# Optimization experiments

Measured on AMD Instinct MI355X. Metric: run time of the kernel, lower is better.

Reference implementation:

```python
import jax, jax.numpy as jnp
import numpy as np

B, T, N, F_, KH, D, KD = 16, 12, 325, 64, 4, 16, 3  # batch, time, nodes, feat, heads, head_dim, diffusion steps
H = KH // 2
EPS = 1e-5


def setup_inputs() -> dict:
    key = jax.random.key(0)
    ks = jax.random.split(key, 16)
    lin = lambda k: (jax.random.normal(k, (F_, F_), jnp.float32) * 0.02)
    return {
        "x": jax.random.normal(ks[0], (B, T, N, F_), jnp.float32),
        "A": jax.random.uniform(ks[1], (KD, N, N), jnp.float32),
        "AT": jax.random.uniform(ks[2], (KD, N, N), jnp.float32),
        "Wq": lin(ks[3]), "bq": jnp.zeros((F_,), jnp.float32),
        "Wk": lin(ks[4]), "bk": jnp.zeros((F_,), jnp.float32),
        "Wks": lin(ks[5]), "bks": jnp.zeros((F_,), jnp.float32),
        "Wv": lin(ks[6]), "bv": jnp.zeros((F_,), jnp.float32),
        "Wvs": lin(ks[7]), "bvs": jnp.zeros((F_,), jnp.float32),
        "Wdi": jax.random.normal(ks[8], (H, KD, N, N), jnp.float32) * 0.05,
        "Wdo": jax.random.normal(ks[9], (H, KD, N, N), jnp.float32) * 0.05,
        "Wf1": lin(ks[10]), "bf1": jnp.zeros((F_,), jnp.float32),
        "Wf2": lin(ks[11]), "bf2": jnp.zeros((F_,), jnp.float32),
        "g_ln": jnp.ones((F_,), jnp.float32), "b_ln": jnp.zeros((F_,), jnp.float32),
    }


def _heads(y):
    # [B,T,N,F] -> [KH,B,T,N,D]  (torch.split along -1 then stack on dim 0)
    return y.reshape(B, T, N, KH, D).transpose(3, 0, 1, 2, 4)


def _attn_half(q, k, ks_, v, vs, bias):
    # q,k,ks_,v,vs: [H,B,T,N,D]; bias: [H,1,1,N,N]
    scale = 1.0 / jnp.sqrt(jnp.float32(D))
    e = jnp.einsum('hbtnd,hbtmd->hbtnm', q, k) * scale + bias
    es = jax.nn.sigmoid((q * ks_).sum(-1, keepdims=True) * scale)  # [H,B,T,N,1]
    e = e - e.max(-1, keepdims=True)
    ex = jnp.exp(e)
    a = ex / (es + ex.sum(-1, keepdims=True))  # sigmoid-augmented softmax
    out = jnp.einsum('hbtnm,hbtmd->hbtnd', a, v)
    return out + vs - a.sum(-1, keepdims=True) * vs


def reference(x, A, AT, Wq, bq, Wk, bk, Wks, bks, Wv, bv, Wvs, bvs,
              Wdi, Wdo, Wf1, bf1, Wf2, bf2, g_ln, b_ln):
    q = _heads(x @ Wq.T + bq)
    k = _heads(x @ Wk.T + bk)
    ks_ = _heads(x @ Wks.T + bks)
    v = _heads(x @ Wv.T + bv)
    vs = _heads(x @ Wvs.T + bvs)

    # DCN graph-diffusion bias: sum_j W[h,j] * A[j] -> [H,1,1,N,N]
    bias_i = jnp.einsum('hknm,knm->hnm', Wdi, A)[:, None, None]
    bias_o = jnp.einsum('hknm,knm->hnm', Wdo, AT)[:, None, None]

    vi = _attn_half(q[:H], k[:H], ks_[:H], v[:H], vs[:H], bias_i)
    vo = _attn_half(q[H:], k[H:], ks_[H:], v[H:], vs[H:], bias_o)

    val = jnp.concatenate([vi, vo], 0)  # [KH,B,T,N,D]
    val = val.transpose(1, 2, 3, 0, 4).reshape(B, T, N, F_)

    h = jax.nn.gelu(val @ Wf1.T + bf1, approximate=False) @ Wf2.T + bf2
    h = h + x

    mu = h.mean(-1, keepdims=True)
    var = ((h - mu) ** 2).mean(-1, keepdims=True)
    return g_ln * (h - mu) / jnp.sqrt(var + EPS) + b_ln
```

## Files before the change

kernel.cpp:

```cpp
#include <hip/hip_runtime.h>
#include <hip/hip_bf16.h>
#include <math.h>

#define NN 325
#define FD 64
#define KH 4
#define DH 16
#define BT 192
#define NN2 (NN*NN)
#define PST (NN*DH)
#define SSTR 340
#define BSTR 352
#define VTS  352
#define VSLICE (16*VTS)
#define HSTR 72
#define NPROJ 975
#define NBIAS ((KH*NN*BSTR + 255)/256)
#define NPAD  (KH*BT)
#define LOG2E 1.44269504088896f

typedef __attribute__((ext_vector_type(8))) short short8;
typedef __attribute__((ext_vector_type(4))) float f32x4;

union U8 { uint4 u; short8 s; ushort us[8]; };
__device__ inline short8 lds8(const ushort* p){ U8 t; t.u = *(const uint4*)p; return t.s; }
__device__ inline float b2f(ushort v){ return __uint_as_float(((unsigned)v) << 16); }
__device__ inline ushort f2b(float f){
  unsigned u = __float_as_uint(f);
  u += 0x7fff + ((u >> 16) & 1);
  return (ushort)(u >> 16);
}
__device__ inline unsigned pk2(float a, float b){
  union { __hip_bfloat162 h; unsigned u; } t;
  t.h = __float22bfloat162_rn(float2{a, b});
  return t.u;
}
__device__ inline short8 cvt8(const float* p){
  float4 u = ((const float4*)p)[0], v = ((const float4*)p)[1];
  U8 t;
  t.us[0]=f2b(u.x); t.us[1]=f2b(u.y); t.us[2]=f2b(u.z); t.us[3]=f2b(u.w);
  t.us[4]=f2b(v.x); t.us[5]=f2b(v.y); t.us[6]=f2b(v.z); t.us[7]=f2b(v.w);
  return t.s;
}

__global__ __launch_bounds__(256) void wpack_kernel(
    const float* __restrict__ Wq,  const float* __restrict__ bq,
    const float* __restrict__ Wk,  const float* __restrict__ bk,
    const float* __restrict__ Wks, const float* __restrict__ bks,
    const float* __restrict__ Wv,  const float* __restrict__ bv,
    const float* __restrict__ Wvs, const float* __restrict__ bvs,
    const float* __restrict__ Wf1, const float* __restrict__ Wf2,
    ushort* __restrict__ Wcat, float* __restrict__ bcat){
  int blk = blockIdx.x;
  const float* Ws[7] = {Wq, Wk, Wks, Wv, Wvs, Wf1, Wf2};
  const float* bs[5] = {bq, bk, bks, bv, bvs};
  int f = blk * 64 + (threadIdx.x >> 2);
  int c0 = (threadIdx.x & 3) * 8;
  const float* wr = Ws[blk] + (f & 63) * 64;
  unsigned* dst = (unsigned*)Wcat + f * 32 + c0;
  #pragma unroll
  for (int c = 0; c < 8; ++c)
    dst[c] = f2b(wr[2*(c0+c)]) | ((unsigned)f2b(wr[2*(c0+c)+1]) << 16);
  if (blk < 5 && (threadIdx.x & 3) == 0) bcat[f] = bs[blk][f & 63];
}

__global__ __launch_bounds__(256) void prep_kernel(
    const float* __restrict__ x, const ushort* __restrict__ Wcat,
    const float* __restrict__ bcat, ushort* __restrict__ proj,
    ushort* __restrict__ vt,
    const float* __restrict__ Wdi, const float* __restrict__ Wdo,
    const float* __restrict__ A,   const float* __restrict__ AT,
    float* __restrict__ biasP){
  int bid = blockIdx.x, tid = threadIdx.x;
  if (bid < NPROJ){
    int lane = tid & 63, wid = tid >> 6;
    int r0 = bid * 64 + wid * 16;
    int m = lane & 15, g = lane >> 4;
    int gr = r0 + m;
    int bt = gr / NN, n = gr - bt * NN;
    const float* xr = x + (size_t)gr * 64 + g * 8;
    short8 xb0 = cvt8(xr);
    short8 xb1 = cvt8(xr + 32);
    for (int ct = 0; ct < 20; ++ct){
      short8 w0 = lds8(Wcat + ((size_t)(ct*16 + m) * 64 + g * 8));
      short8 w1 = lds8(Wcat + ((size_t)(ct*16 + m) * 64 + g * 8 + 32));
      float4 b4 = *(const float4*)(bcat + ct*16 + 4*g);
      f32x4 acc = {b4.x, b4.y, b4.z, b4.w};
      acc = __builtin_amdgcn_mfma_f32_16x16x32_bf16(w0, xb0, acc, 0, 0, 0);
      acc = __builtin_amdgcn_mfma_f32_16x16x32_bf16(w1, xb1, acc, 0, 0, 0);
      if (ct >= 12 && ct < 16){
        ushort* vs = vt + (size_t)((ct-12)*BT + bt) * VSLICE + n;
        #pragma unroll
        for (int rg = 0; rg < 4; ++rg)
          vs[(size_t)(4*g + rg) * VTS] = f2b(acc[rg]);
      } else {
        float sc = (ct < 4) ? 0.25f * LOG2E : 1.0f;
        uint2 w;
        w.x = pk2(acc[0]*sc, acc[1]*sc);
        w.y = pk2(acc[2]*sc, acc[3]*sc);
        *(uint2*)(proj + ((size_t)ct * BT + bt) * PST + n*16 + 4*g) = w;
      }
    }
  } else if (bid < NPROJ + NBIAS){
    int idx = (bid - NPROJ) * 256 + tid;
    if (idx >= KH * NN * BSTR) return;
    int h = idx / (NN * BSTR), rem = idx - h * (NN * BSTR);
    int n = rem / BSTR, m = rem - n * BSTR;
    float s = -1e30f;
    if (m < NN){
      int r = n * NN + m;
      s = 0.f;
      if (h < 2){
        #pragma unroll
        for (int k = 0; k < 3; ++k) s += Wdi[(h*3 + k)*NN2 + r] * A[k*NN2 + r];
      } else {
        int h2 = h - 2;
        #pragma unroll
        for (int k = 0; k < 3; ++k) s += Wdo[(h2*3 + k)*NN2 + r] * AT[k*NN2 + r];
      }
      s *= LOG2E;
    }
    biasP[idx] = s;
  } else {
    int slice = bid - NPROJ - NBIAS;
    ushort* vs = vt + (size_t)slice * VSLICE;
    if (tid < 432){
      int d = tid / 27, c = NN + tid % 27;
      vs[(size_t)d * VTS + c] = 0;
    }
  }
}

__global__ __launch_bounds__(256, 4) void attn_kernel(
    const ushort* __restrict__ proj, const float* __restrict__ biasP,
    const ushort* __restrict__ vt, ushort* __restrict__ val){
  __shared__ float S[16 * SSTR];
  __shared__ float part[4][16][16];
  __shared__ float rstat[16][2];
  int bhid = blockIdx.x, qt = blockIdx.y;
  int h = bhid / BT, bt = bhid - h * BT;
  int tid = threadIdx.x, lane = tid & 63, wid = tid >> 6;
  const ushort* qb  = proj + (size_t)((0*KH + h)*BT + bt) * PST;
  const ushort* kb  = proj + (size_t)((1*KH + h)*BT + bt) * PST;
  const ushort* ksb = proj + (size_t)((2*KH + h)*BT + bt) * PST;
  const ushort* vsb = proj + (size_t)((4*KH + h)*BT + bt) * PST;
  const ushort* vtg = vt + (size_t)(h*BT + bt) * VSLICE;

  int m = lane & 15, g = lane >> 4;
  short8 zero = {0,0,0,0,0,0,0,0};

  short8 aq = (g < 2) ? lds8(qb + ((size_t)(qt*16 + m) * 16 + g * 8)) : zero;
  short8 kf[6];
  #pragma unroll
  for (int i = 0; i < 6; ++i){
    int ct = wid + 4*i;
    kf[i] = (ct < 21 && g < 2) ? lds8(kb + ((size_t)(ct*16 + m) * 16 + g * 8)) : zero;
  }
  short8 vf[3];
  #pragma unroll
  for (int i = 0; i < 3; ++i){
    int tt = wid + 4*i;
    vf[i] = (tt < 11) ? lds8(vtg + (size_t)m * VTS + tt*32 + g*8) : zero;
  }
  int r = tid >> 4, c = tid & 15;
  int n = qt * 16 + r;
  int nb = min(n, NN - 1);
  const float* bp = biasP + (size_t)(h*NN + nb) * BSTR;
  float4 b4[6];
  #pragma unroll
  for (int j = 0; j < 6; ++j){
    int m0 = c * 4 + 64 * j;
    b4[j] = (m0 < 336) ? *(const float4*)(bp + m0) : make_float4(0.f,0.f,0.f,0.f);
  }
  float qv  = b2f(qb[(size_t)nb * 16 + c]);
  float kv  = b2f(ksb[(size_t)nb * 16 + c]);
  float vsv = b2f(vsb[(size_t)nb * 16 + c]);

  #pragma unroll
  for (int i = 0; i < 6; ++i){
    int ct = wid + 4*i;
    if (ct < 21){
      f32x4 acc = {0.f, 0.f, 0.f, 0.f};
      acc = __builtin_amdgcn_mfma_f32_16x16x32_bf16(aq, kf[i], acc, 0, 0, 0);
      #pragma unroll
      for (int rg = 0; rg < 4; ++rg)
        S[(g*4 + rg)*SSTR + ct*16 + m] = acc[rg];
    }
  }
  __syncthreads();

  {
    float* sr = S + r * SSTR;
    ushort* pr = (ushort*)sr;
    float sum = 0.f;
    #pragma unroll
    for (int j = 0; j < 6; ++j){
      int m0 = c * 4 + 64 * j;
      if (m0 < 336){
        float4 s4 = *(const float4*)(sr + m0);
        float e0 = __builtin_amdgcn_exp2f(s4.x + b4[j].x);
        float e1 = __builtin_amdgcn_exp2f(s4.y + b4[j].y);
        float e2 = __builtin_amdgcn_exp2f(s4.z + b4[j].z);
        float e3 = __builtin_amdgcn_exp2f(s4.w + b4[j].w);
        sum += (e0 + e1) + (e2 + e3);
        uint2 w;
        w.x = pk2(e0, e1);
        w.y = pk2(e2, e3);
        *(uint2*)(pr + m0) = w;
      }
    }
    float dp = qv * kv;
    dp += __shfl_xor(dp, 1, 64); dp += __shfl_xor(dp, 2, 64);
    dp += __shfl_xor(dp, 4, 64); dp += __shfl_xor(dp, 8, 64);
    sum += __shfl_xor(sum, 1, 64); sum += __shfl_xor(sum, 2, 64);
    sum += __shfl_xor(sum, 4, 64); sum += __shfl_xor(sum, 8, 64);
    if (c == 0){
      float esv = __builtin_amdgcn_rcpf(1.f + __builtin_amdgcn_exp2f(-dp));
      float iv  = __builtin_amdgcn_rcpf(esv + sum);
      rstat[r][0] = iv; rstat[r][1] = 1.f - sum * iv;
    }
  }
  __syncthreads();

  {
    const ushort* prow = (const ushort*)S + (size_t)m * (SSTR * 2);
    f32x4 acc = {0.f, 0.f, 0.f, 0.f};
    #pragma unroll
    for (int i = 0; i < 3; ++i){
      int tt = wid + 4*i;
      if (tt < 11){
        short8 ap = (tt == 10 && g >= 2) ? zero : lds8(prow + tt*32 + g*8);
        acc = __builtin_amdgcn_mfma_f32_16x16x32_bf16(ap, vf[i], acc, 0, 0, 0);
      }
    }
    #pragma unroll
    for (int rg = 0; rg < 4; ++rg)
      part[wid][g*4 + rg][m] = acc[rg];
  }
  __syncthreads();

  if (n < NN){
    float s = part[0][r][c] + part[1][r][c] + part[2][r][c] + part[3][r][c];
    float res = s * rstat[r][0] + rstat[r][1] * vsv;
    val[((size_t)bt * NN + n) * FD + h * 16 + c] = f2b(res);
  }
}

__global__ __launch_bounds__(256) void ffn_kernel(
    const ushort* __restrict__ val, const float* __restrict__ x,
    const ushort* __restrict__ Wf1b, const float* __restrict__ bf1,
    const ushort* __restrict__ Wf2b, const float* __restrict__ bf2,
    const float* __restrict__ g_ln, const float* __restrict__ b_ln,
    float* __restrict__ out){
  __shared__ ushort hs[4][16 * HSTR];
  int tid = threadIdx.x, lane = tid & 63, wid = tid >> 6;
  int m = lane & 15, g = lane >> 4;
  int r0 = blockIdx.x * 64 + wid * 16;
  int row = r0 + m;

  short8 vb0 = lds8(val + ((size_t)row * 64 + g * 8));
  short8 vb1 = lds8(val + ((size_t)row * 64 + g * 8 + 32));

  #pragma unroll
  for (int ct = 0; ct < 4; ++ct){
    short8 w0 = lds8(Wf1b + ((size_t)(ct*16 + m) * 64 + g * 8));
    short8 w1 = lds8(Wf1b + ((size_t)(ct*16 + m) * 64 + g * 8 + 32));
    float4 b4 = *(const float4*)(bf1 + ct*16 + 4*g);
    f32x4 acc = {b4.x, b4.y, b4.z, b4.w};
    acc = __builtin_amdgcn_mfma_f32_16x16x32_bf16(w0, vb0, acc, 0, 0, 0);
    acc = __builtin_amdgcn_mfma_f32_16x16x32_bf16(w1, vb1, acc, 0, 0, 0);
    uint2 w;
    float g0 = 0.5f*acc[0]*(1.f + erff(acc[0]*0.70710678118654752f));
    float g1 = 0.5f*acc[1]*(1.f + erff(acc[1]*0.70710678118654752f));
    float g2 = 0.5f*acc[2]*(1.f + erff(acc[2]*0.70710678118654752f));
    float g3 = 0.5f*acc[3]*(1.f + erff(acc[3]*0.70710678118654752f));
    w.x = pk2(g0, g1); w.y = pk2(g2, g3);
    *(uint2*)&hs[wid][m * HSTR + ct*16 + 4*g] = w;
  }
  asm volatile("s_waitcnt lgkmcnt(0)" ::: "memory");
  short8 h0 = lds8(&hs[wid][m * HSTR + g * 8]);
  short8 h1 = lds8(&hs[wid][m * HSTR + g * 8 + 32]);

  float t[4][4];
  #pragma unroll
  for (int ct = 0; ct < 4; ++ct){
    short8 w0 = lds8(Wf2b + ((size_t)(ct*16 + m) * 64 + g * 8));
    short8 w1 = lds8(Wf2b + ((size_t)(ct*16 + m) * 64 + g * 8 + 32));
    float4 b4 = *(const float4*)(bf2 + ct*16 + 4*g);
    f32x4 acc = {b4.x, b4.y, b4.z, b4.w};
    acc = __builtin_amdgcn_mfma_f32_16x16x32_bf16(w0, h0, acc, 0, 0, 0);
    acc = __builtin_amdgcn_mfma_f32_16x16x32_bf16(w1, h1, acc, 0, 0, 0);
    float4 xr = *(const float4*)(x + (size_t)row * 64 + ct*16 + 4*g);
    t[ct][0] = acc[0] + xr.x; t[ct][1] = acc[1] + xr.y;
    t[ct][2] = acc[2] + xr.z; t[ct][3] = acc[3] + xr.w;
  }
  float s = 0.f;
  #pragma unroll
  for (int ct = 0; ct < 4; ++ct) s += (t[ct][0]+t[ct][1]) + (t[ct][2]+t[ct][3]);
  s += __shfl_xor(s, 16, 64); s += __shfl_xor(s, 32, 64);
  float mu = s * (1.f/64.f);
  float v = 0.f;
  #pragma unroll
  for (int ct = 0; ct < 4; ++ct){
    #pragma unroll
    for (int rg = 0; rg < 4; ++rg){ float d = t[ct][rg] - mu; v += d*d; }
  }
  v += __shfl_xor(v, 16, 64); v += __shfl_xor(v, 32, 64);
  float rs = rsqrtf(v * (1.f/64.f) + 1e-5f);
  #pragma unroll
  for (int ct = 0; ct < 4; ++ct){
    float4 g4 = *(const float4*)(g_ln + ct*16 + 4*g);
    float4 bb = *(const float4*)(b_ln + ct*16 + 4*g);
    float4 o;
    o.x = g4.x*(t[ct][0]-mu)*rs + bb.x;
    o.y = g4.y*(t[ct][1]-mu)*rs + bb.y;
    o.z = g4.z*(t[ct][2]-mu)*rs + bb.z;
    o.w = g4.w*(t[ct][3]-mu)*rs + bb.w;
    *(float4*)(out + (size_t)row * 64 + ct*16 + 4*g) = o;
  }
}

extern "C" void kernel_launch(void* const* d_in, const int* in_sizes, int n_in,
                              void* d_out, int out_size, void* d_ws, size_t ws_size,
                              hipStream_t stream) {
  const float* x    = (const float*)d_in[0];
  const float* A    = (const float*)d_in[1];
  const float* AT   = (const float*)d_in[2];
  const float* Wq   = (const float*)d_in[3];
  const float* bq   = (const float*)d_in[4];
  const float* Wk   = (const float*)d_in[5];
  const float* bk   = (const float*)d_in[6];
  const float* Wks  = (const float*)d_in[7];
  const float* bks  = (const float*)d_in[8];
  const float* Wv   = (const float*)d_in[9];
  const float* bv   = (const float*)d_in[10];
  const float* Wvs  = (const float*)d_in[11];
  const float* bvs  = (const float*)d_in[12];
  const float* Wdi  = (const float*)d_in[13];
  const float* Wdo  = (const float*)d_in[14];
  const float* Wf1  = (const float*)d_in[15];
  const float* bf1  = (const float*)d_in[16];
  const float* Wf2  = (const float*)d_in[17];
  const float* bf2  = (const float*)d_in[18];
  const float* g_ln = (const float*)d_in[19];
  const float* b_ln = (const float*)d_in[20];
  float* out = (float*)d_out;

  float* ws = (float*)d_ws;
  ushort* proj  = (ushort*)ws;
  float*  biasP = ws + 9984000;
  ushort* val   = (ushort*)(ws + 10441600);
  ushort* vt    = (ushort*)(ws + 12438400);
  ushort* Wcat  = (ushort*)(ws + 14601088);
  float*  bcat  = ws + 14615424;
  ushort* Wf1b  = Wcat + 320*64;
  ushort* Wf2b  = Wcat + 384*64;

  wpack_kernel<<<7, 256, 0, stream>>>(Wq, bq, Wk, bk, Wks, bks,
                                      Wv, bv, Wvs, bvs, Wf1, Wf2, Wcat, bcat);
  prep_kernel<<<NPROJ + NBIAS + NPAD, 256, 0, stream>>>(
      x, Wcat, bcat, proj, vt, Wdi, Wdo, A, AT, biasP);
  attn_kernel<<<dim3(KH*BT, 21), 256, 0, stream>>>(proj, biasP, vt, val);
  ffn_kernel<<<975, 256, 0, stream>>>(val, x, Wf1b, bf1, Wf2b, bf2,
                                      g_ln, b_ln, out);
}
```

Measured before the change: 198.1 us.

## Rewrite attention as single-wave blocks with transposed bias and compacted projections

The attention kernel goes from four waves per block, with three barriers and a cross-wave reduction, to one 64-thread wave per block. That wave loops over all 21 key tiles, applies exp2 to the MFMA output in registers, writes bf16 probabilities to LDS and keeps row sums in registers. The diffusion bias is now written transposed (336x336 per head) through a shared-memory tile transpose, so each lane reads a float4 that matches its MFMA output layout. The projection buffer also drops the unused value slots, which shrinks the workspace. The aim is to remove barrier and LDS round-trip overhead. The cost is less parallelism per block, serial per-wave loops, and K and V loaded directly from global memory inside the loop.

```diff
diff --git a/kernel.cpp b/kernel.cpp
--- a/kernel.cpp
+++ b/kernel.cpp
@@ -9,13 +9,14 @@
 #define BT 192
 #define NN2 (NN*NN)
 #define PST (NN*DH)
-#define SSTR 340
-#define BSTR 352
+#define BTN 336
+#define BTH (336*336)
 #define VTS  352
 #define VSLICE (16*VTS)
+#define PSTR 344
 #define HSTR 72
 #define NPROJ 975
-#define NBIAS ((KH*NN*BSTR + 255)/256)
+#define NBIAS 144
 #define NPAD  (KH*BT)
 #define LOG2E 1.44269504088896f
 
@@ -70,7 +71,8 @@
     ushort* __restrict__ vt,
     const float* __restrict__ Wdi, const float* __restrict__ Wdo,
     const float* __restrict__ A,   const float* __restrict__ AT,
-    float* __restrict__ biasP){
+    float* __restrict__ biasT){
+  __shared__ float tile[64 * 65];
   int bid = blockIdx.x, tid = threadIdx.x;
   if (bid < NPROJ){
     int lane = tid & 63, wid = tid >> 6;
@@ -94,33 +96,51 @@
         for (int rg = 0; rg < 4; ++rg)
           vs[(size_t)(4*g + rg) * VTS] = f2b(acc[rg]);
       } else {
+        int slot = (ct < 12) ? ct : ct - 4;
         float sc = (ct < 4) ? 0.25f * LOG2E : 1.0f;
         uint2 w;
         w.x = pk2(acc[0]*sc, acc[1]*sc);
         w.y = pk2(acc[2]*sc, acc[3]*sc);
-        *(uint2*)(proj + ((size_t)ct * BT + bt) * PST + n*16 + 4*g) = w;
+        *(uint2*)(proj + ((size_t)slot * BT + bt) * PST + n*16 + 4*g) = w;
       }
     }
   } else if (bid < NPROJ + NBIAS){
-    int idx = (bid - NPROJ) * 256 + tid;
-    if (idx >= KH * NN * BSTR) return;
-    int h = idx / (NN * BSTR), rem = idx - h * (NN * BSTR);
-    int n = rem / BSTR, m = rem - n * BSTR;
-    float s = -1e30f;
-    if (m < NN){
-      int r = n * NN + m;
-      s = 0.f;
-      if (h < 2){
-        #pragma unroll
-        for (int k = 0; k < 3; ++k) s += Wdi[(h*3 + k)*NN2 + r] * A[k*NN2 + r];
-      } else {
-        int h2 = h - 2;
-        #pragma unroll
-        for (int k = 0; k < 3; ++k) s += Wdo[(h2*3 + k)*NN2 + r] * AT[k*NN2 + r];
+    int tb = bid - NPROJ;
+    int h = tb / 36, rem = tb - h * 36;
+    int nt = rem / 6, mt = rem - nt * 6;
+    int n0 = nt * 64, m0 = mt * 64;
+    #pragma unroll
+    for (int i = 0; i < 16; ++i){
+      int idx = i * 256 + tid;
+      int nn = idx >> 6, mm = idx & 63;
+      int n = n0 + nn, mc = m0 + mm;
+      float s;
+      if (mc >= NN) s = -1e30f;
+      else if (n >= NN) s = 0.f;
+      else {
+        int r = n * NN + mc;
+        s = 0.f;
+        if (h < 2){
+          #pragma unroll
+          for (int k = 0; k < 3; ++k) s += Wdi[(h*3 + k)*NN2 + r] * A[k*NN2 + r];
+        } else {
+          int h2 = h - 2;
+          #pragma unroll
+          for (int k = 0; k < 3; ++k) s += Wdo[(h2*3 + k)*NN2 + r] * AT[k*NN2 + r];
+        }
+        s *= LOG2E;
       }
-      s *= LOG2E;
-    }
-    biasP[idx] = s;
+      tile[mm * 65 + nn] = s;
+    }
+    __syncthreads();
+    #pragma unroll
+    for (int i = 0; i < 16; ++i){
+      int idx = i * 256 + tid;
+      int mm = idx >> 6, nn = idx & 63;
+      int gm = m0 + mm, gn = n0 + nn;
+      if (gm < BTN && gn < BTN)
+        biasT[(size_t)h * BTH + (size_t)gm * BTN + gn] = tile[mm * 65 + nn];
+    }
   } else {
     int slice = bid - NPROJ - NBIAS;
     ushort* vs = vt + (size_t)slice * VSLICE;
@@ -131,118 +151,81 @@
   }
 }
 
-__global__ __launch_bounds__(256, 4) void attn_kernel(
-    const ushort* __restrict__ proj, const float* __restrict__ biasP,
+__global__ __launch_bounds__(64) void attn_kernel(
+    const ushort* __restrict__ proj, const float* __restrict__ biasT,
     const ushort* __restrict__ vt, ushort* __restrict__ val){
-  __shared__ float S[16 * SSTR];
-  __shared__ float part[4][16][16];
-  __shared__ float rstat[16][2];
+  __shared__ ushort P[16 * PSTR];
   int bhid = blockIdx.x, qt = blockIdx.y;
   int h = bhid / BT, bt = bhid - h * BT;
-  int tid = threadIdx.x, lane = tid & 63, wid = tid >> 6;
-  const ushort* qb  = proj + (size_t)((0*KH + h)*BT + bt) * PST;
-  const ushort* kb  = proj + (size_t)((1*KH + h)*BT + bt) * PST;
-  const ushort* ksb = proj + (size_t)((2*KH + h)*BT + bt) * PST;
-  const ushort* vsb = proj + (size_t)((4*KH + h)*BT + bt) * PST;
+  int lane = threadIdx.x & 63;
+  int m = lane & 15, g = lane >> 4;
+  const ushort* qb  = proj + (size_t)(( 0 + h)*BT + bt) * PST;
+  const ushort* kb  = proj + (size_t)(( 4 + h)*BT + bt) * PST;
+  const ushort* ksb = proj + (size_t)(( 8 + h)*BT + bt) * PST;
+  const ushort* vsb = proj + (size_t)((12 + h)*BT + bt) * PST;
   const ushort* vtg = vt + (size_t)(h*BT + bt) * VSLICE;
-
-  int m = lane & 15, g = lane >> 4;
   short8 zero = {0,0,0,0,0,0,0,0};
 
   short8 aq = (g < 2) ? lds8(qb + ((size_t)(qt*16 + m) * 16 + g * 8)) : zero;
-  short8 kf[6];
-  #pragma unroll
-  for (int i = 0; i < 6; ++i){
-    int ct = wid + 4*i;
-    kf[i] = (ct < 21 && g < 2) ? lds8(kb + ((size_t)(ct*16 + m) * 16 + g * 8)) : zero;
-  }
-  short8 vf[3];
-  #pragma unroll
-  for (int i = 0; i < 3; ++i){
-    int tt = wid + 4*i;
-    vf[i] = (tt < 11) ? lds8(vtg + (size_t)m * VTS + tt*32 + g*8) : zero;
-  }
-  int r = tid >> 4, c = tid & 15;
-  int n = qt * 16 + r;
-  int nb = min(n, NN - 1);
-  const float* bp = biasP + (size_t)(h*NN + nb) * BSTR;
-  float4 b4[6];
-  #pragma unroll
-  for (int j = 0; j < 6; ++j){
-    int m0 = c * 4 + 64 * j;
-    b4[j] = (m0 < 336) ? *(const float4*)(bp + m0) : make_float4(0.f,0.f,0.f,0.f);
-  }
-  float qv  = b2f(qb[(size_t)nb * 16 + c]);
-  float kv  = b2f(ksb[(size_t)nb * 16 + c]);
-  float vsv = b2f(vsb[(size_t)nb * 16 + c]);
-
-  #pragma unroll
-  for (int i = 0; i < 6; ++i){
-    int ct = wid + 4*i;
-    if (ct < 21){
-      f32x4 acc = {0.f, 0.f, 0.f, 0.f};
-      acc = __builtin_amdgcn_mfma_f32_16x16x32_bf16(aq, kf[i], acc, 0, 0, 0);
-      #pragma unroll
-      for (int rg = 0; rg < 4; ++rg)
-        S[(g*4 + rg)*SSTR + ct*16 + m] = acc[rg];
-    }
-  }
-  __syncthreads();
-
-  {
-    float* sr = S + r * SSTR;
-    ushort* pr = (ushort*)sr;
-    float sum = 0.f;
+  float qv[4], kv[4], vsv[4];
+  #pragma unroll
+  for (int rg = 0; rg < 4; ++rg){
+    int nn = min(qt*16 + g*4 + rg, NN - 1);
+    qv[rg]  = b2f(qb [(size_t)nn * 16 + m]);
+    kv[rg]  = b2f(ksb[(size_t)nn * 16 + m]);
+    vsv[rg] = b2f(vsb[(size_t)nn * 16 + m]);
+  }
+
+  const float* bTc = biasT + (size_t)h * BTH + qt*16 + g*4;
+  float sm[4] = {0.f, 0.f, 0.f, 0.f};
+  for (int ct = 0; ct < 21; ++ct){
+    int col = ct*16 + m;
+    short8 kf = (g < 2) ? lds8(kb + ((size_t)col * 16 + g * 8)) : zero;
+    f32x4 s = {0.f, 0.f, 0.f, 0.f};
+    s = __builtin_amdgcn_mfma_f32_16x16x32_bf16(aq, kf, s, 0, 0, 0);
+    float4 b4 = *(const float4*)(bTc + (size_t)col * BTN);
+    float e0 = __builtin_amdgcn_exp2f(s[0] + b4.x);
+    float e1 = __builtin_amdgcn_exp2f(s[1] + b4.y);
+    float e2 = __builtin_amdgcn_exp2f(s[2] + b4.z);
+    float e3 = __builtin_amdgcn_exp2f(s[3] + b4.w);
+    sm[0] += e0; sm[1] += e1; sm[2] += e2; sm[3] += e3;
+    P[(g*4 + 0) * PSTR + col] = f2b(e0);
+    P[(g*4 + 1) * PSTR + col] = f2b(e1);
+    P[(g*4 + 2) * PSTR + col] = f2b(e2);
+    P[(g*4 + 3) * PSTR + col] = f2b(e3);
+  }
+
+  float dp[4];
+  #pragma unroll
+  for (int rg = 0; rg < 4; ++rg) dp[rg] = qv[rg] * kv[rg];
+  #pragma unroll
+  for (int o = 1; o <= 8; o <<= 1){
     #pragma unroll
-    for (int j = 0; j < 6; ++j){
-      int m0 = c * 4 + 64 * j;
-      if (m0 < 336){
-        float4 s4 = *(const float4*)(sr + m0);
-        float e0 = __builtin_amdgcn_exp2f(s4.x + b4[j].x);
-        float e1 = __builtin_amdgcn_exp2f(s4.y + b4[j].y);
-        float e2 = __builtin_amdgcn_exp2f(s4.z + b4[j].z);
-        float e3 = __builtin_amdgcn_exp2f(s4.w + b4[j].w);
-        sum += (e0 + e1) + (e2 + e3);
-        uint2 w;
-        w.x = pk2(e0, e1);
-        w.y = pk2(e2, e3);
-        *(uint2*)(pr + m0) = w;
-      }
-    }
-    float dp = qv * kv;
-    dp += __shfl_xor(dp, 1, 64); dp += __shfl_xor(dp, 2, 64);
-    dp += __shfl_xor(dp, 4, 64); dp += __shfl_xor(dp, 8, 64);
-    sum += __shfl_xor(sum, 1, 64); sum += __shfl_xor(sum, 2, 64);
-    sum += __shfl_xor(sum, 4, 64); sum += __shfl_xor(sum, 8, 64);
-    if (c == 0){
-      float esv = __builtin_amdgcn_rcpf(1.f + __builtin_amdgcn_exp2f(-dp));
-      float iv  = __builtin_amdgcn_rcpf(esv + sum);
-      rstat[r][0] = iv; rstat[r][1] = 1.f - sum * iv;
-    }
-  }
-  __syncthreads();
-
-  {
-    const ushort* prow = (const ushort*)S + (size_t)m * (SSTR * 2);
-    f32x4 acc = {0.f, 0.f, 0.f, 0.f};
-    #pragma unroll
-    for (int i = 0; i < 3; ++i){
-      int tt = wid + 4*i;
-      if (tt < 11){
-        short8 ap = (tt == 10 && g >= 2) ? zero : lds8(prow + tt*32 + g*8);
-        acc = __builtin_amdgcn_mfma_f32_16x16x32_bf16(ap, vf[i], acc, 0, 0, 0);
-      }
-    }
-    #pragma unroll
-    for (int rg = 0; rg < 4; ++rg)
-      part[wid][g*4 + rg][m] = acc[rg];
-  }
-  __syncthreads();
-
-  if (n < NN){
-    float s = part[0][r][c] + part[1][r][c] + part[2][r][c] + part[3][r][c];
-    float res = s * rstat[r][0] + rstat[r][1] * vsv;
-    val[((size_t)bt * NN + n) * FD + h * 16 + c] = f2b(res);
+    for (int rg = 0; rg < 4; ++rg){
+      sm[rg] += __shfl_xor(sm[rg], o, 64);
+      dp[rg] += __shfl_xor(dp[rg], o, 64);
+    }
+  }
+
+  asm volatile("s_waitcnt lgkmcnt(0)" ::: "memory");
+  const ushort* prow = P + (size_t)m * PSTR;
+  f32x4 acc = {0.f, 0.f, 0.f, 0.f};
+  #pragma unroll
+  for (int tt = 0; tt < 11; ++tt){
+    short8 ap = (tt == 10 && g >= 2) ? zero : lds8(prow + tt*32 + g*8);
+    short8 bv = lds8(vtg + (size_t)m * VTS + tt*32 + g*8);
+    acc = __builtin_amdgcn_mfma_f32_16x16x32_bf16(ap, bv, acc, 0, 0, 0);
+  }
+
+  #pragma unroll
+  for (int rg = 0; rg < 4; ++rg){
+    int n = qt*16 + g*4 + rg;
+    if (n < NN){
+      float esv = __builtin_amdgcn_rcpf(1.f + __builtin_amdgcn_exp2f(-dp[rg]));
+      float iv  = __builtin_amdgcn_rcpf(esv + sm[rg]);
+      float res = acc[rg] * iv + (1.f - sm[rg] * iv) * vsv[rg];
+      val[((size_t)bt * NN + n) * FD + h*16 + m] = f2b(res);
+    }
   }
 }
 
@@ -348,19 +331,19 @@
 
   float* ws = (float*)d_ws;
   ushort* proj  = (ushort*)ws;
-  float*  biasP = ws + 9984000;
-  ushort* val   = (ushort*)(ws + 10441600);
-  ushort* vt    = (ushort*)(ws + 12438400);
-  ushort* Wcat  = (ushort*)(ws + 14601088);
-  float*  bcat  = ws + 14615424;
+  float*  biasT = ws + 7987200;
+  ushort* val   = (ushort*)(ws + 8438784);
+  ushort* vt    = (ushort*)(ws + 10435584);
+  ushort* Wcat  = (ushort*)(ws + 12598272);
+  float*  bcat  = ws + 12612608;
   ushort* Wf1b  = Wcat + 320*64;
   ushort* Wf2b  = Wcat + 384*64;
 
   wpack_kernel<<<7, 256, 0, stream>>>(Wq, bq, Wk, bk, Wks, bks,
                                       Wv, bv, Wvs, bvs, Wf1, Wf2, Wcat, bcat);
   prep_kernel<<<NPROJ + NBIAS + NPAD, 256, 0, stream>>>(
-      x, Wcat, bcat, proj, vt, Wdi, Wdo, A, AT, biasP);
-  attn_kernel<<<dim3(KH*BT, 21), 256, 0, stream>>>(proj, biasP, vt, val);
+      x, Wcat, bcat, proj, vt, Wdi, Wdo, A, AT, biasT);
+  attn_kernel<<<dim3(KH*BT, 21), 64, 0, stream>>>(proj, biasT, vt, val);
   ffn_kernel<<<975, 256, 0, stream>>>(val, x, Wf1b, bf1, Wf2b, bf2,
                                       g_ln, b_ln, out);
 }
```

New measurement: 212.8 us. 1.07x slower.
